# Kernel tuning notes

Measured on AMD Instinct MI355X. Metric: run time of the kernel, lower is better.

The kernel has to match this reference:

```python
import jax, jax.numpy as jnp
import numpy as np

I, H, L, O = 128, 512, 2, 1  # input_size, hidden_size, num_layers, output_size
B, S = 64, 512


def setup_inputs() -> dict:
    key = jax.random.key(0)
    ks = jax.random.split(key, 12)
    inp = {
        "x": jax.random.normal(ks[0], (B, S, I), dtype=jnp.float32),
        "theta": jax.random.normal(ks[1], (I, H), dtype=jnp.float32) * 0.02,
        "phi": jax.random.normal(ks[2], (I, H), dtype=jnp.float32) * 0.02,
        "theta_noise": jax.random.normal(ks[3], (I, H), dtype=jnp.float32) * 0.01,
        "phi_noise": jax.random.normal(ks[4], (I, H), dtype=jnp.float32) * 0.01,
        # stacked per-layer LSTM weights (all layers take H-dim input)
        "W_ih": jax.random.normal(ks[5], (L, 4 * H, H), dtype=jnp.float32) * (1.0 / np.sqrt(H)),
        "W_hh": jax.random.normal(ks[6], (L, 4 * H, H), dtype=jnp.float32) * (1.0 / np.sqrt(H)),
        "b_ih": jax.random.normal(ks[7], (L, 4 * H), dtype=jnp.float32) * (1.0 / np.sqrt(H)),
        "b_hh": jax.random.normal(ks[8], (L, 4 * H), dtype=jnp.float32) * (1.0 / np.sqrt(H)),
        "fc1_w": jax.random.normal(ks[9], (H, H), dtype=jnp.float32) * (1.0 / np.sqrt(H)),
        "fc1_b": jnp.zeros((H,), dtype=jnp.float32),
        "fc2_w": jax.random.normal(ks[10], (O, H), dtype=jnp.float32) * (1.0 / np.sqrt(H)),
        "fc2_b": jnp.zeros((O,), dtype=jnp.float32),
    }
    return inp


def _lstm_layer(xs, Wih, Whh, bih, bhh):
    # xs: (S, B, H) -> hs: (S, B, H). PyTorch gate order: i, f, g, o.
    Bn = xs.shape[1]
    Hn = Whh.shape[1]
    # precompute input projections for all timesteps in one GEMM
    x_proj = jnp.einsum("sbh,gh->sbg", xs, Wih) + bih + bhh  # (S, B, 4H)

    def step(carry, xp):
        h, c = carry
        gates = xp + h @ Whh.T  # (B, 4H)
        i, f, g, o = jnp.split(gates, 4, axis=-1)
        i = jax.nn.sigmoid(i)
        f = jax.nn.sigmoid(f)
        g = jnp.tanh(g)
        o = jax.nn.sigmoid(o)
        c = f * c + i * g
        h = o * jnp.tanh(c)
        return (h, c), h

    h0 = jnp.zeros((Bn, Hn), dtype=xs.dtype)
    c0 = jnp.zeros((Bn, Hn), dtype=xs.dtype)
    _, hs = jax.lax.scan(step, (h0, c0), x_proj)
    return hs


def reference(x, theta, phi, theta_noise, phi_noise, W_ih, W_hh, b_ih, b_hh,
              fc1_w, fc1_b, fc2_w, fc2_b):
    # QuantumInspiredLayer: |x @ (cos(theta+n) + i*sin(phi+n))| done as two real GEMMs
    real = jnp.einsum("bsi,ih->bsh", x, jnp.cos(theta + theta_noise))
    imag = jnp.einsum("bsi,ih->bsh", x, jnp.sin(phi + phi_noise))
    q = jnp.sqrt(real * real + imag * imag)  # (B, S, H)

    hs = jnp.transpose(q, (1, 0, 2))  # (S, B, H)
    n_layers = W_ih.shape[0]
    for l in range(n_layers):
        hs = _lstm_layer(hs, W_ih[l], W_hh[l], b_ih[l], b_hh[l])
    last = hs[-1]  # (B, H) -- out[:, -1, :]

    h1 = jax.nn.relu(last @ fc1_w.T + fc1_b)
    # dropout is identity in eval mode
    return h1 @ fc2_w.T + fc2_b  # (B, O)
```

## Files before the change

### kernel.cpp

```cpp
#include <hip/hip_runtime.h>


typedef _Float16 f16;
typedef _Float16 f16x8 __attribute__((ext_vector_type(8)));
typedef float f32x4 __attribute__((ext_vector_type(4)));
typedef unsigned long long u64;

#define MFMA16(a, b, c) __builtin_amdgcn_mfma_f32_16x16x32_f16((a), (b), (c), 0, 0, 0)
#define LD_AG(p) __hip_atomic_load((p), __ATOMIC_RELAXED, __HIP_MEMORY_SCOPE_AGENT)
#define ST_AG(p, v) __hip_atomic_store((p), (v), __ATOMIC_RELAXED, __HIP_MEMORY_SCOPE_AGENT)

#define OFF_Q16 0UL
#define OFF_X16 33554432UL
#define OFF_W16 41943040UL
#define OFF_COS 50331648UL
#define OFF_SIN 50462720UL
#define OFF_BSUM 50593792UL
#define OFF_H1 50610176UL
#define OFF_HLAST 50741248UL
#define OFF_FC1WT 50872320UL
#define OFF_FLG 51920896UL
#define OFF_H0 51953664UL
#define WS_NEEDED 85573632UL

__global__ __launch_bounds__(256) void k_prep(
    const float* __restrict__ x, const float* __restrict__ theta,
    const float* __restrict__ phi, const float* __restrict__ thn,
    const float* __restrict__ phn, const float* __restrict__ Wih,
    const float* __restrict__ Whh, const float* __restrict__ bih,
    const float* __restrict__ bhh, const float* __restrict__ fc1w,
    f16* __restrict__ x16, f16* __restrict__ w16, f16* __restrict__ cosT,
    f16* __restrict__ sinT, float* __restrict__ bsum, float* __restrict__ fc1wT,
    f16* __restrict__ h0buf, f16* __restrict__ h1buf, unsigned* __restrict__ flg) {
  const int T1 = 4194304;
  const int T2 = T1 + 4194304;
  const int T3 = T2 + 65536;
  const int T4 = T3 + 262144;
  const int T5 = T4 + 4096;
  const int T6 = T5 + 98304;
  const int T7 = T6 + 8192;
  for (int idx = blockIdx.x * 256 + threadIdx.x; idx < T7; idx += gridDim.x * 256) {
    if (idx < T1) {
      int s = idx >> 13, rem = idx & 8191, b = rem >> 7, i = rem & 127;
      x16[idx] = (f16)x[b * 65536 + s * 128 + i];
    } else if (idx < T2) {
      int j = idx - T1;
      int l = j >> 21, rem = j & 2097151, r = rem >> 10, k = rem & 1023;
      float v = (k < 512) ? Wih[((size_t)l * 2048 + r) * 512 + k]
                          : Whh[((size_t)l * 2048 + r) * 512 + (k - 512)];
      w16[(size_t)l * 2097152 + (size_t)r * 1024 + k] = (f16)v;
    } else if (idx < T3) {
      int e = idx - T2;
      int i = e >> 9, h = e & 511;
      cosT[h * 128 + i] = (f16)cosf(theta[e] + thn[e]);
      sinT[h * 128 + i] = (f16)sinf(phi[e] + phn[e]);
    } else if (idx < T4) {
      int e = idx - T3;
      int n = e >> 9, k = e & 511;
      fc1wT[k * 512 + n] = fc1w[e];
    } else if (idx < T5) {
      int e = idx - T4;
      bsum[e] = bih[e] + bhh[e];
    } else if (idx < T6) {
      int e = idx - T5;
      if (e < 65536) {
        h1buf[e] = (f16)0.f;
      } else {
        int e2 = e - 65536;
        int dm = e2 >> 13, o = e2 & 8191;
        h0buf[(size_t)dm * 513 * 8192 + o] = (f16)0.f;
      }
    } else {
      flg[idx - T6] = 0u;
    }
  }
}

__global__ __launch_bounds__(256) void k_quantum(
    const f16* __restrict__ x16, const f16* __restrict__ cosT,
    const f16* __restrict__ sinT, f16* __restrict__ q16) {
  __shared__ __align__(16) f16 a_lds[64 * 136];
  const int tid = threadIdx.x;
  const int r0 = blockIdx.x * 64, h0 = blockIdx.y * 128;
#pragma unroll
  for (int g = 0; g < 4; ++g) {
    int G = g * 256 + tid, row = G >> 4, col = G & 15;
    *(uint4*)((char*)a_lds + row * 272 + col * 16) =
        *(const uint4*)(x16 + (size_t)(r0 + row) * 128 + col * 8);
  }
  __syncthreads();
  const int wv = tid >> 6, lane = tid & 63, n15 = lane & 15, quad = lane >> 4;
  const int nb = h0 + wv * 32;
  f32x4 ac[4][2], as_[4][2];
#pragma unroll
  for (int mt = 0; mt < 4; ++mt)
#pragma unroll
    for (int nt = 0; nt < 2; ++nt) {
      ac[mt][nt] = (f32x4){0.f, 0.f, 0.f, 0.f};
      as_[mt][nt] = (f32x4){0.f, 0.f, 0.f, 0.f};
    }
#pragma unroll
  for (int it = 0; it < 4; ++it) {
    f16x8 a[4];
#pragma unroll
    for (int mt = 0; mt < 4; ++mt)
      a[mt] = *(const f16x8*)((const char*)a_lds + (mt * 16 + n15) * 272 + it * 64 + quad * 16);
#pragma unroll
    for (int nt = 0; nt < 2; ++nt) {
      const f16x8 bc = *(const f16x8*)(cosT + (size_t)(nb + nt * 16 + n15) * 128 + it * 32 + quad * 8);
      const f16x8 bs = *(const f16x8*)(sinT + (size_t)(nb + nt * 16 + n15) * 128 + it * 32 + quad * 8);
#pragma unroll
      for (int mt = 0; mt < 4; ++mt) {
        ac[mt][nt] = MFMA16(a[mt], bc, ac[mt][nt]);
        as_[mt][nt] = MFMA16(a[mt], bs, as_[mt][nt]);
      }
    }
  }
#pragma unroll
  for (int mt = 0; mt < 4; ++mt)
#pragma unroll
    for (int nt = 0; nt < 2; ++nt)
#pragma unroll
      for (int r = 0; r < 4; ++r) {
        int row = r0 + mt * 16 + quad * 4 + r;
        int col = nb + nt * 16 + n15;
        float re = ac[mt][nt][r], im = as_[mt][nt][r];
        q16[(size_t)row * 512 + col] = (f16)sqrtf(re * re + im * im);
      }
}

__device__ __forceinline__ f16x8 lds_a(const char* astage, int row, int it, int quad) {
  int pos = (it * 4 + quad) ^ (row & 7);
  return *(const f16x8*)(astage + row * 2048 + pos * 16);
}
__device__ __forceinline__ float sigf(float x) { return 1.f / (1.f + __expf(-x)); }
__device__ __forceinline__ float tanhf_fast(float x) { return 1.f - 2.f / (__expf(2.f * x) + 1.f); }

__global__ __launch_bounds__(512, 2) void k_rec(
    const f16* __restrict__ q16, const f16* __restrict__ w16,
    const float* __restrict__ bsum, f16* __restrict__ h0buf,
    f16* __restrict__ h1buf, float* __restrict__ hlast, unsigned* flg) {
  __shared__ __align__(16) char astage[32768];
  __shared__ float gbuf[16 * 132];

  const int tid = threadIdx.x, lane = tid & 63, wv = tid >> 6;
  const int n15 = lane & 15, quad = lane >> 4;
  const int qg = wv >> 1, ch = wv & 1;
  const int dom = blockIdx.x >> 5, role = blockIdx.x & 31;
  const int l = role >> 4, c0 = (role & 15) * 32;
  const int b0 = dom * 16;

  f16x8 wf[32];
  {
    const f16* wbase = w16 + ((size_t)l * 2048 + (size_t)(qg * 512 + c0 + ch * 16 + n15)) * 1024 + quad * 8;
#pragma unroll
    for (int it = 0; it < 32; ++it) wf[it] = *(const f16x8*)(wbase + it * 32);
  }
  float bb[4][2];
#pragma unroll
  for (int g = 0; g < 4; ++g)
#pragma unroll
    for (int j = 0; j < 2; ++j)
      bb[g][j] = bsum[l * 2048 + g * 512 + c0 + (tid & 15) * 2 + j];
  float cs0 = 0.f, cs1 = 0.f;

  unsigned* f0 = flg + (size_t)(dom * 2 + 0) * 1024;
  unsigned* f1 = flg + (size_t)(dom * 2 + 1) * 1024;
  unsigned* myflag = (l ? f1 : f0) + (size_t)(role & 15) * 64;
  const unsigned* pollp;
  if (l == 0) pollp = f0 + (size_t)(lane & 15) * 64;
  else pollp = (lane < 32) ? (f0 + (size_t)(lane & 15) * 64)
                           : (f1 + (size_t)(lane & 15) * 64);

  const int srow = tid >> 5, scg = tid & 31;
  const int g0 = scg * 2;
  char* a_x0 = astage + srow * 2048 + ((g0 ^ (srow & 7)) * 16);
  char* a_x1 = astage + srow * 2048 + (((g0 + 1) ^ (srow & 7)) * 16);
  char* a_h0 = a_x0 + 1024;
  char* a_h1 = a_x1 + 1024;
  const size_t soff = (size_t)srow * 512 + scg * 16;
  const size_t h0base = (size_t)dom * 513 * 8192;
  const size_t h1base = (size_t)dom * 2 * 8192;

  for (int t = 0; t <= 511; ++t) {
    if (l == 0) {
      const f16* src = q16 + ((size_t)(t * 64 + b0 + srow)) * 512 + scg * 16;
      uint4 v0 = *(const uint4*)src;
      uint4 v1 = *(const uint4*)(src + 8);
      *(uint4*)a_x0 = v0;
      *(uint4*)a_x1 = v1;
    }
    if (l == 0) {
      if (t >= 1) {
        while (true) {
          int f = (int)LD_AG(pollp);
          if (__all(f >= t)) break;
        }
      }
    } else {
      const int mytgt = (lane < 32) ? (t + 1) : t;
      while (true) {
        int f = (int)LD_AG(pollp);
        if (__all(f >= mytgt)) break;
      }
    }
    if (l == 0) {
      const u64* hs0 = (const u64*)(h0buf + h0base + (size_t)t * 8192 + soff);
      u64 x0 = LD_AG(hs0);
      u64 x1 = LD_AG(hs0 + 1);
      u64 x2 = LD_AG(hs0 + 2);
      u64 x3 = LD_AG(hs0 + 3);
      ((u64*)a_h0)[0] = x0; ((u64*)a_h0)[1] = x1;
      ((u64*)a_h1)[0] = x2; ((u64*)a_h1)[1] = x3;
    } else {
      const u64* hs0 = (const u64*)(h0buf + h0base + (size_t)(t + 1) * 8192 + soff);
      u64 x0 = LD_AG(hs0);
      u64 x1 = LD_AG(hs0 + 1);
      u64 x2 = LD_AG(hs0 + 2);
      u64 x3 = LD_AG(hs0 + 3);
      const u64* hs1 = (const u64*)(h1buf + h1base + (size_t)((t - 1) & 1) * 8192 + soff);
      u64 y0 = LD_AG(hs1);
      u64 y1 = LD_AG(hs1 + 1);
      u64 y2 = LD_AG(hs1 + 2);
      u64 y3 = LD_AG(hs1 + 3);
      ((u64*)a_x0)[0] = x0; ((u64*)a_x0)[1] = x1;
      ((u64*)a_x1)[0] = x2; ((u64*)a_x1)[1] = x3;
      ((u64*)a_h0)[0] = y0; ((u64*)a_h0)[1] = y1;
      ((u64*)a_h1)[0] = y2; ((u64*)a_h1)[1] = y3;
    }
    __syncthreads();

    f32x4 acca = (f32x4){0.f, 0.f, 0.f, 0.f};
    f32x4 accb = (f32x4){0.f, 0.f, 0.f, 0.f};
#pragma unroll
    for (int it = 0; it < 16; ++it) {
      acca = MFMA16(lds_a(astage, n15, 2 * it, quad), wf[2 * it], acca);
      accb = MFMA16(lds_a(astage, n15, 2 * it + 1, quad), wf[2 * it + 1], accb);
    }
#pragma unroll
    for (int r = 0; r < 4; ++r)
      gbuf[(quad * 4 + r) * 132 + qg * 33 + ch * 16 + n15] = acca[r] + accb[r];
    __syncthreads();

    if (tid < 256) {
      const int b = tid >> 4, jc = (tid & 15) * 2;
      float hv[2];
#pragma unroll
      for (int j = 0; j < 2; ++j) {
        const float* gb = gbuf + b * 132 + jc + j;
        float gi = gb[0] + bb[0][j];
        float gf = gb[33] + bb[1][j];
        float gg = gb[66] + bb[2][j];
        float go = gb[99] + bb[3][j];
        float cprev = j ? cs1 : cs0;
        float c = sigf(gf) * cprev + sigf(gi) * tanhf_fast(gg);
        if (j) cs1 = c; else cs0 = c;
        hv[j] = sigf(go) * tanhf_fast(c);
      }
      union { f16 h2[2]; unsigned u; } pk;
      pk.h2[0] = (f16)hv[0];
      pk.h2[1] = (f16)hv[1];
      f16* dst = (l == 0)
          ? h0buf + h0base + (size_t)(t + 1) * 8192 + (size_t)b * 512 + c0 + jc
          : h1buf + h1base + (size_t)(t & 1) * 8192 + (size_t)b * 512 + c0 + jc;
      ST_AG((unsigned*)dst, pk.u);
      if (l == 1 && t == 511) {
        hlast[(size_t)(b0 + b) * 512 + c0 + jc] = hv[0];
        hlast[(size_t)(b0 + b) * 512 + c0 + jc + 1] = hv[1];
      }
    }
    __syncthreads();
    if (tid == 0) ST_AG(myflag, (unsigned)(t + 1));
  }
}

__global__ __launch_bounds__(512) void k_fc(
    const float* __restrict__ hlast, const float* __restrict__ fc1wT,
    const float* __restrict__ fc1b, const float* __restrict__ fc2w,
    const float* __restrict__ fc2b, float* __restrict__ out) {
  __shared__ float hrow[512];
  __shared__ float red[8];
  const int b = blockIdx.x, tid = threadIdx.x;
  hrow[tid] = hlast[b * 512 + tid];
  __syncthreads();
  float acc = 0.f;
#pragma unroll 8
  for (int k = 0; k < 512; ++k) acc += hrow[k] * fc1wT[k * 512 + tid];
  float h1 = acc + fc1b[tid];
  h1 = h1 > 0.f ? h1 : 0.f;
  float v = h1 * fc2w[tid];
#pragma unroll
  for (int off = 32; off >= 1; off >>= 1) v += __shfl_down(v, off);
  if ((tid & 63) == 0) red[tid >> 6] = v;
  __syncthreads();
  if (tid == 0) {
    float s = 0.f;
#pragma unroll
    for (int w = 0; w < 8; ++w) s += red[w];
    out[b] = s + fc2b[0];
  }
}

extern "C" void kernel_launch(void* const* d_in, const int* in_sizes, int n_in,
                              void* d_out, int out_size, void* d_ws, size_t ws_size,
                              hipStream_t stream) {
  if (ws_size < WS_NEEDED) return;

  const float* x = (const float*)d_in[0];
  const float* theta = (const float*)d_in[1];
  const float* phi = (const float*)d_in[2];
  const float* thn = (const float*)d_in[3];
  const float* phn = (const float*)d_in[4];
  const float* Wih = (const float*)d_in[5];
  const float* Whh = (const float*)d_in[6];
  const float* bih = (const float*)d_in[7];
  const float* bhh = (const float*)d_in[8];
  const float* fc1w = (const float*)d_in[9];
  const float* fc1b = (const float*)d_in[10];
  const float* fc2w = (const float*)d_in[11];
  const float* fc2b = (const float*)d_in[12];

  char* ws = (char*)d_ws;
  f16* q16 = (f16*)(ws + OFF_Q16);
  f16* x16 = (f16*)(ws + OFF_X16);
  f16* w16 = (f16*)(ws + OFF_W16);
  f16* cosT = (f16*)(ws + OFF_COS);
  f16* sinT = (f16*)(ws + OFF_SIN);
  float* bsum = (float*)(ws + OFF_BSUM);
  f16* h1buf = (f16*)(ws + OFF_H1);
  f16* h0buf = (f16*)(ws + OFF_H0);
  float* hlast = (float*)(ws + OFF_HLAST);
  float* fc1wT = (float*)(ws + OFF_FC1WT);
  unsigned* flg = (unsigned*)(ws + OFF_FLG);

  k_prep<<<2048, 256, 0, stream>>>(x, theta, phi, thn, phn, Wih, Whh, bih, bhh, fc1w,
                                   x16, w16, cosT, sinT, bsum, fc1wT, h0buf, h1buf, flg);
  k_quantum<<<dim3(512, 4, 1), 256, 0, stream>>>(x16, cosT, sinT, q16);
  k_rec<<<128, 512, 0, stream>>>(q16, w16, bsum, h0buf, h1buf, hlast, flg);
  k_fc<<<64, 512, 0, stream>>>(hlast, fc1wT, fc1b, fc2w, fc2b, (float*)d_out);
}
```

Baseline: 1.936 ms.

## Replace flag polling with step-tagged hidden-state words in ring buffers

The recurrent kernel now stores each f16 hidden value in a 32-bit word whose upper half holds the timestep tag. Consumers spin directly on the data until every tag matches, which removes the separate flag store and poll and the trailing __syncthreads per step. Hidden states move into small ring buffers (8 slots for layer 0, 4 for layer 1). Only layer 1 still publishes a progress flag, so layer 0 cannot overrun the ring. This halves the useful payload per load and adds tag-checking work, and the ring depth caps how far layer 0 can run ahead of layer 1.

```diff
diff --git a/kernel.cpp b/kernel.cpp
--- a/kernel.cpp
+++ b/kernel.cpp
@@ -16,12 +16,12 @@
 #define OFF_COS 50331648UL
 #define OFF_SIN 50462720UL
 #define OFF_BSUM 50593792UL
-#define OFF_H1 50610176UL
-#define OFF_HLAST 50741248UL
-#define OFF_FC1WT 50872320UL
-#define OFF_FLG 51920896UL
-#define OFF_H0 51953664UL
-#define WS_NEEDED 85573632UL
+#define OFF_HLAST 50610176UL
+#define OFF_FC1WT 50741248UL
+#define OFF_FLG 51789824UL
+#define OFF_H0R 51806208UL
+#define OFF_H1R 52854784UL
+#define WS_NEEDED 53379072UL
 
 __global__ __launch_bounds__(256) void k_prep(
     const float* __restrict__ x, const float* __restrict__ theta,
@@ -31,14 +31,15 @@
     const float* __restrict__ bhh, const float* __restrict__ fc1w,
     f16* __restrict__ x16, f16* __restrict__ w16, f16* __restrict__ cosT,
     f16* __restrict__ sinT, float* __restrict__ bsum, float* __restrict__ fc1wT,
-    f16* __restrict__ h0buf, f16* __restrict__ h1buf, unsigned* __restrict__ flg) {
+    unsigned* __restrict__ h0r, unsigned* __restrict__ h1r,
+    unsigned* __restrict__ flg) {
   const int T1 = 4194304;
   const int T2 = T1 + 4194304;
   const int T3 = T2 + 65536;
   const int T4 = T3 + 262144;
   const int T5 = T4 + 4096;
-  const int T6 = T5 + 98304;
-  const int T7 = T6 + 8192;
+  const int T6 = T5 + 65536;
+  const int T7 = T6 + 4096;
   for (int idx = blockIdx.x * 256 + threadIdx.x; idx < T7; idx += gridDim.x * 256) {
     if (idx < T1) {
       int s = idx >> 13, rem = idx & 8191, b = rem >> 7, i = rem & 127;
@@ -63,12 +64,13 @@
       bsum[e] = bih[e] + bhh[e];
     } else if (idx < T6) {
       int e = idx - T5;
-      if (e < 65536) {
-        h1buf[e] = (f16)0.f;
+      if (e < 32768) {
+        int dm = e >> 13, o = e & 8191;
+        h0r[(size_t)dm * 65536 + o] = 0u;
       } else {
-        int e2 = e - 65536;
+        int e2 = e - 32768;
         int dm = e2 >> 13, o = e2 & 8191;
-        h0buf[(size_t)dm * 513 * 8192 + o] = (f16)0.f;
+        h1r[(size_t)dm * 32768 + o] = 0u;
       }
     } else {
       flg[idx - T6] = 0u;
@@ -135,11 +137,30 @@
 }
 __device__ __forceinline__ float sigf(float x) { return 1.f / (1.f + __expf(-x)); }
 __device__ __forceinline__ float tanhf_fast(float x) { return 1.f - 2.f / (__expf(2.f * x) + 1.f); }
+__device__ __forceinline__ bool tags_ok(const unsigned* v, unsigned tgt) {
+  unsigned m = 0;
+#pragma unroll
+  for (int i = 0; i < 16; ++i) m |= (v[i] >> 16) ^ tgt;
+  return m == 0;
+}
+__device__ __forceinline__ void unpack_lds(const unsigned* v, char* d0, char* d1) {
+  uint4 a, b;
+  a.x = (v[0] & 0xFFFFu) | (v[1] << 16);
+  a.y = (v[2] & 0xFFFFu) | (v[3] << 16);
+  a.z = (v[4] & 0xFFFFu) | (v[5] << 16);
+  a.w = (v[6] & 0xFFFFu) | (v[7] << 16);
+  b.x = (v[8] & 0xFFFFu) | (v[9] << 16);
+  b.y = (v[10] & 0xFFFFu) | (v[11] << 16);
+  b.z = (v[12] & 0xFFFFu) | (v[13] << 16);
+  b.w = (v[14] & 0xFFFFu) | (v[15] << 16);
+  *(uint4*)d0 = a;
+  *(uint4*)d1 = b;
+}
 
 __global__ __launch_bounds__(512, 2) void k_rec(
     const f16* __restrict__ q16, const f16* __restrict__ w16,
-    const float* __restrict__ bsum, f16* __restrict__ h0buf,
-    f16* __restrict__ h1buf, float* __restrict__ hlast, unsigned* flg) {
+    const float* __restrict__ bsum, unsigned* __restrict__ h0r,
+    unsigned* __restrict__ h1r, float* __restrict__ hlast, unsigned* flg) {
   __shared__ __align__(16) char astage[32768];
   __shared__ float gbuf[16 * 132];
 
@@ -164,13 +185,10 @@
       bb[g][j] = bsum[l * 2048 + g * 512 + c0 + (tid & 15) * 2 + j];
   float cs0 = 0.f, cs1 = 0.f;
 
-  unsigned* f0 = flg + (size_t)(dom * 2 + 0) * 1024;
-  unsigned* f1 = flg + (size_t)(dom * 2 + 1) * 1024;
-  unsigned* myflag = (l ? f1 : f0) + (size_t)(role & 15) * 64;
-  const unsigned* pollp;
-  if (l == 0) pollp = f0 + (size_t)(lane & 15) * 64;
-  else pollp = (lane < 32) ? (f0 + (size_t)(lane & 15) * 64)
-                           : (f1 + (size_t)(lane & 15) * 64);
+  unsigned* f1 = flg + (size_t)dom * 1024;
+  unsigned* myf1 = f1 + (size_t)(role & 15) * 64;
+  const unsigned* g1p = f1 + (size_t)(lane & 15) * 64;
+  unsigned g1v = LD_AG(g1p);
 
   const int srow = tid >> 5, scg = tid & 31;
   const int g0 = scg * 2;
@@ -178,9 +196,9 @@
   char* a_x1 = astage + srow * 2048 + (((g0 + 1) ^ (srow & 7)) * 16);
   char* a_h0 = a_x0 + 1024;
   char* a_h1 = a_x1 + 1024;
-  const size_t soff = (size_t)srow * 512 + scg * 16;
-  const size_t h0base = (size_t)dom * 513 * 8192;
-  const size_t h1base = (size_t)dom * 2 * 8192;
+  const size_t soff32 = (size_t)srow * 512 + scg * 16;
+  const size_t h0dom = (size_t)dom * 8 * 8192;
+  const size_t h1dom = (size_t)dom * 4 * 8192;
 
   for (int t = 0; t <= 511; ++t) {
     if (l == 0) {
@@ -191,42 +209,38 @@
       *(uint4*)a_x1 = v1;
     }
     if (l == 0) {
-      if (t >= 1) {
-        while (true) {
-          int f = (int)LD_AG(pollp);
-          if (__all(f >= t)) break;
+      const unsigned* s0 = h0r + h0dom + (size_t)(t & 7) * 8192 + soff32;
+      unsigned hv0[16];
+      bool dn = false;
+      while (true) {
+        if (!dn) {
+#pragma unroll
+          for (int i = 0; i < 16; ++i) hv0[i] = LD_AG(s0 + i);
+          dn = tags_ok(hv0, (unsigned)t);
         }
-      }
+        if (__all((int)dn)) break;
+      }
+      unpack_lds(hv0, a_h0, a_h1);
     } else {
-      const int mytgt = (lane < 32) ? (t + 1) : t;
+      const unsigned* s0 = h0r + h0dom + (size_t)((t + 1) & 7) * 8192 + soff32;
+      const unsigned* s1 = h1r + h1dom + (size_t)(t & 3) * 8192 + soff32;
+      unsigned hv0[16], hv1[16];
+      bool d0 = false, d1 = false;
       while (true) {
-        int f = (int)LD_AG(pollp);
-        if (__all(f >= mytgt)) break;
-      }
-    }
-    if (l == 0) {
-      const u64* hs0 = (const u64*)(h0buf + h0base + (size_t)t * 8192 + soff);
-      u64 x0 = LD_AG(hs0);
-      u64 x1 = LD_AG(hs0 + 1);
-      u64 x2 = LD_AG(hs0 + 2);
-      u64 x3 = LD_AG(hs0 + 3);
-      ((u64*)a_h0)[0] = x0; ((u64*)a_h0)[1] = x1;
-      ((u64*)a_h1)[0] = x2; ((u64*)a_h1)[1] = x3;
-    } else {
-      const u64* hs0 = (const u64*)(h0buf + h0base + (size_t)(t + 1) * 8192 + soff);
-      u64 x0 = LD_AG(hs0);
-      u64 x1 = LD_AG(hs0 + 1);
-      u64 x2 = LD_AG(hs0 + 2);
-      u64 x3 = LD_AG(hs0 + 3);
-      const u64* hs1 = (const u64*)(h1buf + h1base + (size_t)((t - 1) & 1) * 8192 + soff);
-      u64 y0 = LD_AG(hs1);
-      u64 y1 = LD_AG(hs1 + 1);
-      u64 y2 = LD_AG(hs1 + 2);
-      u64 y3 = LD_AG(hs1 + 3);
-      ((u64*)a_x0)[0] = x0; ((u64*)a_x0)[1] = x1;
-      ((u64*)a_x1)[0] = x2; ((u64*)a_x1)[1] = x3;
-      ((u64*)a_h0)[0] = y0; ((u64*)a_h0)[1] = y1;
-      ((u64*)a_h1)[0] = y2; ((u64*)a_h1)[1] = y3;
+        if (!d0) {
+#pragma unroll
+          for (int i = 0; i < 16; ++i) hv0[i] = LD_AG(s0 + i);
+          d0 = tags_ok(hv0, (unsigned)(t + 1));
+        }
+        if (!d1) {
+#pragma unroll
+          for (int i = 0; i < 16; ++i) hv1[i] = LD_AG(s1 + i);
+          d1 = tags_ok(hv1, (unsigned)t);
+        }
+        if (__all((int)(d0 && d1))) break;
+      }
+      unpack_lds(hv0, a_x0, a_x1);
+      unpack_lds(hv1, a_h0, a_h1);
     }
     __syncthreads();
 
@@ -241,6 +255,12 @@
     for (int r = 0; r < 4; ++r)
       gbuf[(quad * 4 + r) * 132 + qg * 33 + ch * 16 + n15] = acca[r] + accb[r];
     __syncthreads();
+
+    if (l == 0 && t >= 7) {
+      const int need = t - 7;
+      while ((int)g1v < need) g1v = LD_AG(g1p);
+      g1v = LD_AG(g1p);
+    }
 
     if (tid < 256) {
       const int b = tid >> 4, jc = (tid & 15) * 2;
@@ -257,20 +277,21 @@
         if (j) cs1 = c; else cs0 = c;
         hv[j] = sigf(go) * tanhf_fast(c);
       }
-      union { f16 h2[2]; unsigned u; } pk;
-      pk.h2[0] = (f16)hv[0];
-      pk.h2[1] = (f16)hv[1];
-      f16* dst = (l == 0)
-          ? h0buf + h0base + (size_t)(t + 1) * 8192 + (size_t)b * 512 + c0 + jc
-          : h1buf + h1base + (size_t)(t & 1) * 8192 + (size_t)b * 512 + c0 + jc;
-      ST_AG((unsigned*)dst, pk.u);
+      union { f16 h; unsigned short s; } u0, u1;
+      u0.h = (f16)hv[0];
+      u1.h = (f16)hv[1];
+      const unsigned tag = (unsigned)(t + 1) << 16;
+      u64 pk = (u64)(tag | u0.s) | ((u64)(tag | u1.s) << 32);
+      unsigned* dst = (l == 0)
+          ? h0r + h0dom + (size_t)((t + 1) & 7) * 8192 + (size_t)b * 512 + c0 + jc
+          : h1r + h1dom + (size_t)((t + 1) & 3) * 8192 + (size_t)b * 512 + c0 + jc;
+      ST_AG((u64*)dst, pk);
       if (l == 1 && t == 511) {
         hlast[(size_t)(b0 + b) * 512 + c0 + jc] = hv[0];
         hlast[(size_t)(b0 + b) * 512 + c0 + jc + 1] = hv[1];
       }
     }
-    __syncthreads();
-    if (tid == 0) ST_AG(myflag, (unsigned)(t + 1));
+    if (l == 1 && tid == 0) ST_AG(myf1, (unsigned)(t + 1));
   }
 }
 
@@ -327,15 +348,15 @@
   f16* cosT = (f16*)(ws + OFF_COS);
   f16* sinT = (f16*)(ws + OFF_SIN);
   float* bsum = (float*)(ws + OFF_BSUM);
-  f16* h1buf = (f16*)(ws + OFF_H1);
-  f16* h0buf = (f16*)(ws + OFF_H0);
   float* hlast = (float*)(ws + OFF_HLAST);
   float* fc1wT = (float*)(ws + OFF_FC1WT);
   unsigned* flg = (unsigned*)(ws + OFF_FLG);
+  unsigned* h0r = (unsigned*)(ws + OFF_H0R);
+  unsigned* h1r = (unsigned*)(ws + OFF_H1R);
 
   k_prep<<<2048, 256, 0, stream>>>(x, theta, phi, thn, phn, Wih, Whh, bih, bhh, fc1w,
-                                   x16, w16, cosT, sinT, bsum, fc1wT, h0buf, h1buf, flg);
+                                   x16, w16, cosT, sinT, bsum, fc1wT, h0r, h1r, flg);
   k_quantum<<<dim3(512, 4, 1), 256, 0, stream>>>(x16, cosT, sinT, q16);
-  k_rec<<<128, 512, 0, stream>>>(q16, w16, bsum, h0buf, h1buf, hlast, flg);
+  k_rec<<<128, 512, 0, stream>>>(q16, w16, bsum, h0r, h1r, hlast, flg);
   k_fc<<<64, 512, 0, stream>>>(hlast, fc1wT, fc1b, fc2w, fc2b, (float*)d_out);
 }
```

New measurement: 6.139 ms. 3.17x slower.
